# Kernel optimization log

Measured on AMD Instinct MI355X. Metric: run time of the kernel, lower is better.

Reference implementation:

```python
import jax, jax.numpy as jnp
import numpy as np
from jax import lax

B, T, NI = 1024, 16, 11

def skew(v):  # [...,3,1] -> [...,3,3]
    x, y, z = v[..., 0, 0], v[..., 1, 0], v[..., 2, 0]
    o = jnp.zeros_like(x)
    return jnp.stack([jnp.stack([o, -z, y], -1),
                      jnp.stack([z, o, -x], -1),
                      jnp.stack([-y, x, o], -1)], -2)

def exp_SO3(phi):  # [...,3,1] -> [...,3,3] (Rodrigues, safe small-angle)
    t2 = jnp.sum(phi * phi, axis=(-2, -1))[..., None, None]
    small = t2 < 1e-8
    t2s = jnp.where(small, 1.0, t2)
    t = jnp.sqrt(t2s)
    A = jnp.where(small, 1.0 - t2 / 6.0, jnp.sin(t) / t)
    Bc = jnp.where(small, 0.5 - t2 / 24.0, (1.0 - jnp.cos(t)) / t2s)
    K = skew(phi)
    return jnp.eye(3, dtype=phi.dtype) + A * K + Bc * (K @ K)

def log_SO3(C):  # [...,3,3] -> [...,3,1]
    tr = jnp.trace(C, axis1=-2, axis2=-1)[..., None, None]
    c = jnp.clip((tr - 1.0) * 0.5, -1.0 + 1e-7, 1.0 - 1e-7)
    t = jnp.arccos(c)
    small = t < 1e-4
    s = jnp.where(small, 1.0, jnp.sin(t))
    coef = jnp.where(small, 0.5 + t * t / 12.0, t / (2.0 * s))
    S = coef * (C - jnp.swapaxes(C, -1, -2))
    return jnp.stack([S[..., 2, 1], S[..., 0, 2], S[..., 1, 0]], -1)[..., None]

def J_left_inv(phi):  # inverse left Jacobian of SO(3)
    t2 = jnp.sum(phi * phi, axis=(-2, -1))[..., None, None]
    small = t2 < 1e-8
    t2s = jnp.where(small, 1.0, t2)
    t = jnp.sqrt(t2s)
    coef = jnp.where(small, 1.0 / 12.0,
                     1.0 / t2s - (1.0 + jnp.cos(t)) / (2.0 * t * jnp.sin(t)))
    K = skew(phi)
    return jnp.eye(3, dtype=phi.dtype) - 0.5 * K + coef * (K @ K)

def decode(s):
    b = s.shape[0]
    return (s[:, 0:3].reshape(b, 3, 1), s[:, 3:12].reshape(b, 3, 3),
            s[:, 12:15].reshape(b, 3, 1), s[:, 15:18].reshape(b, 3, 1),
            s[:, 18:21].reshape(b, 3, 1), s[:, 21:24].reshape(b, 3, 1),
            s[:, 24].reshape(b, 1, 1))

def encode(g, C, r, v, bw, ba, lambd):
    b = g.shape[0]
    return jnp.concatenate([g.reshape(b, 3), C.reshape(b, 9), r.reshape(b, 3),
                            v.reshape(b, 3), bw.reshape(b, 3), ba.reshape(b, 3),
                            lambd.reshape(b, 1)], -1)

def force_sym(M):
    u = jnp.triu(M)
    return u + jnp.swapaxes(u, -1, -2) * (1.0 - jnp.eye(M.shape[-1], dtype=M.dtype))

def predict_one_step(t_acc, C_acc, r_acc, v_acc, dt, g_k, v_k, bw_k, ba_k, covar, gyro, accel, Rimu):
    b = dt.shape[0]
    dt2 = dt * dt
    w = gyro - bw_k
    w_sk = skew(w)
    C_T = jnp.swapaxes(C_acc, -1, -2)
    a = accel - ba_k
    v = C_T @ (v_k - g_k * t_acc + v_acc)
    v_sk = skew(v)
    I3 = jnp.eye(3, dtype=dt.dtype)
    E = exp_SO3(dt * w)
    E_T = jnp.swapaxes(E, -1, -2)
    F = jnp.zeros((b, 19, 19), dt.dtype)
    F = F.at[:, 3:6, 3:6].set(-w_sk)
    F = F.at[:, 3:6, 12:15].set(-I3)
    F = F.at[:, 6:9, 3:6].set(-(C_acc @ v_sk))
    F = F.at[:, 6:9, 9:12].set(C_acc)
    F = F.at[:, 9:12, 0:3].set(-C_T)
    F = F.at[:, 9:12, 3:6].set(-skew(C_T @ g_k))
    F = F.at[:, 9:12, 9:12].set(-w_sk)
    F = F.at[:, 9:12, 12:15].set(-v_sk)
    F = F.at[:, 9:12, 15:18].set(-I3)
    G = jnp.zeros((b, 19, 12), dt.dtype)
    G = G.at[:, 3:6, 0:3].set(-I3)
    G = G.at[:, 9:12, 0:3].set(-v_sk)
    G = G.at[:, 9:12, 6:9].set(-I3)
    G = G.at[:, 12:15, 3:6].set(I3)
    G = G.at[:, 15:18, 9:12].set(I3)
    Phi = jnp.eye(19, dtype=dt.dtype) + F * dt + 0.5 * (F @ F) * dt2
    Phi = Phi.at[:, 6:9, 12:15].set(0.0)
    Phi = Phi.at[:, 3:6, 3:6].set(E_T)
    Phi = Phi.at[:, 9:12, 9:12].set(E_T)
    PhiG = Phi @ G
    Q = (PhiG @ Rimu @ jnp.swapaxes(PhiG, -1, -2)) * dt
    covar = force_sym(Phi @ covar @ jnp.swapaxes(Phi, -1, -2) + Q)
    r_acc = r_acc + v_acc * dt + 0.5 * (C_acc @ (dt2 * a))
    v_acc = v_acc + C_acc @ (dt * a)
    C_acc = C_acc @ E
    t_acc = t_acc + dt
    return t_acc, C_acc, r_acc, v_acc, covar

def predict(imu_meas, Rimu, prev_state, prev_covar):
    b = imu_meas.shape[0]
    dtype = prev_covar.dtype
    g_k, _, _, v_k, bw_k, ba_k, lambd = decode(prev_state)
    u = jnp.array([1.0] * 3 + [0.0] * 6 + [1.0] * 10, dtype)
    covar = prev_covar * (u[:, None] * u[None, :])  # U P U^T with diagonal U
    t = imu_meas[..., 0]
    gyro = imu_meas[..., 1:4][..., None]
    accel = imu_meas[..., 4:7][..., None]
    dt = (t[:, 1:] - t[:, :-1])[..., None, None]
    init = (jnp.zeros((b, 1, 1), dtype),
            jnp.tile(jnp.eye(3, dtype=dtype), (b, 1, 1)),
            jnp.zeros((b, 3, 1), dtype), jnp.zeros((b, 3, 1), dtype), covar)
    xs = (jnp.swapaxes(dt, 0, 1), jnp.swapaxes(gyro[:, :-1], 0, 1), jnp.swapaxes(accel[:, :-1], 0, 1))
    def step(c, x):
        t_acc, C_acc, r_acc, v_acc, cov = c
        dt_, gy, ac = x
        return predict_one_step(t_acc, C_acc, r_acc, v_acc, dt_, g_k, v_k, bw_k, ba_k, cov, gy, ac, Rimu), None
    (t_acc, C_acc, r_acc, v_acc, cov), _ = lax.scan(step, init, xs)
    pred_state = encode(g_k, C_acc,
                        v_k * t_acc - 0.5 * g_k * t_acc * t_acc + r_acc,
                        jnp.swapaxes(C_acc, -1, -2) @ (v_k - g_k * t_acc + v_acc),
                        bw_k, ba_k, lambd)
    return pred_state, cov

def update(pred_state, pred_covar, vis_meas, vis_meas_covar):
    b = pred_state.shape[0]
    dtype = pred_state.dtype
    g_p, C_p, r_p, v_p, bw_p, ba_p, l_p = decode(pred_state)
    phi = log_SO3(C_p)
    residual = jnp.concatenate([vis_meas[:, 0:3] - phi, vis_meas[:, 3:6] - l_p * r_p], 1)
    H = jnp.zeros((b, 6, 19), dtype)
    H = H.at[:, 0:3, 3:6].set(-J_left_inv(-phi))
    H = H.at[:, 3:6, 6:9].set(-jnp.eye(3, dtype=dtype) * l_p)
    H = H.at[:, 3:6, 18:19].set(-r_p)
    H = -H
    H_T = jnp.swapaxes(H, -1, -2)
    S = H @ pred_covar @ H_T + vis_meas_covar
    K = pred_covar @ H_T @ jnp.linalg.inv(S)
    e = K @ residual
    est_covar = (jnp.eye(19, dtype=dtype) - K @ H) @ pred_covar
    est_state = encode(g_p + e[:, 0:3], C_p @ exp_SO3(e[:, 3:6]), r_p + e[:, 6:9],
                       v_p + e[:, 9:12], bw_p + e[:, 12:15], ba_p + e[:, 15:18],
                       l_p + e[:, 18:19])
    return est_state, est_covar

def composition(prev_pose, est_state, est_covar):
    b = est_state.shape[0]
    dtype = est_state.dtype
    g, C, r, v, bw, ba, lambd = decode(est_state)
    C_T = jnp.swapaxes(C, -1, -2)
    pose = jnp.tile(jnp.eye(4, dtype=dtype), (b, 1, 1))
    pose = pose.at[:, 0:3, 0:3].set(C_T @ prev_pose[:, 0:3, 0:3])
    pose = pose.at[:, 0:3, 3:4].set(C_T @ (prev_pose[:, 0:3, 3:4] - r))
    new_g = C_T @ g
    new_state = encode(new_g, C, r, v, bw, ba, lambd)
    U = jnp.tile(jnp.eye(19, dtype=dtype), (b, 1, 1))
    U = U.at[:, 0:3, 0:3].set(C_T)
    U = U.at[:, 0:3, 3:6].set(skew(new_g))
    new_covar = force_sym(U @ est_covar @ jnp.swapaxes(U, -1, -2))
    return pose, new_state, new_covar

def setup_inputs() -> dict:
    key = jax.random.key(0)
    k1, k2, k3 = jax.random.split(key, 3)
    dtype = jnp.float32
    times = jnp.broadcast_to(jnp.arange(NI, dtype=dtype) * 0.01, (B, T, NI))
    gyro = jax.random.normal(k1, (B, T, NI, 3), dtype) * 0.05
    accel = jax.random.normal(k2, (B, T, NI, 3), dtype) * 0.1
    imu_data = jnp.concatenate([times[..., None], gyro, accel], -1)  # [B,T,NI,7]
    imu_noise_covar = jnp.eye(12, dtype=dtype) * 1e-4
    prev_pose = jnp.tile(jnp.eye(4, dtype=dtype), (B, 1, 1))
    g0 = jnp.array([0.0, 0.0, 9.81], dtype)
    C0 = jnp.eye(3, dtype=dtype).reshape(9)
    prev_state = jnp.broadcast_to(
        jnp.concatenate([g0, C0, jnp.zeros(12, dtype), jnp.ones(1, dtype)]), (B, 25))
    prev_covar = jnp.tile(jnp.eye(19, dtype=dtype) * 1e-2, (B, 1, 1))
    vis_meas = jax.random.normal(k3, (B, T, 6, 1), dtype) * 0.01
    vis_meas_covar = jnp.tile(jnp.eye(6, dtype=dtype) * 1e-2, (B, T, 1, 1))
    T_imu_cam = jnp.tile(jnp.eye(4, dtype=dtype), (B, 1, 1))
    return dict(imu_data=imu_data, imu_noise_covar=imu_noise_covar, prev_pose=prev_pose,
                prev_state=prev_state, prev_covar=prev_covar, vis_meas=vis_meas,
                vis_meas_covar=vis_meas_covar, T_imu_cam=T_imu_cam)

def reference(imu_data, imu_noise_covar, prev_pose, prev_state, prev_covar, vis_meas, vis_meas_covar, T_imu_cam):
    num_timesteps = vis_meas.shape[1]
    poses, states, covars = [prev_pose], [prev_state], [prev_covar]
    for k in range(num_timesteps):
        ps, pc = predict(imu_data[:, k], imu_noise_covar, states[-1], covars[-1])
        es, ec = update(ps, pc, vis_meas[:, k], vis_meas_covar[:, k])
        npo, ns, nc = composition(poses[-1], es, ec)
        poses.append(npo); states.append(ns); covars.append(nc)
    return (jnp.stack(poses, 1), jnp.stack(states, 1), jnp.stack(covars, 1))
```

## Files before the change

### kernel.cpp

```cpp
#include <hip/hip_runtime.h>

#define NB 1024
#define NT 16
#define NIM 11
#define PIT 20
#define NTH 128

struct __align__(16) SharedBlob {
    float P0[19*PIT];
    float P1[19*PIT];
    float A9[9*PIT];
    float Dall[10][9*PIT];
    float Wsall[10][9*12];
    float Wu[19*12];
    float Mu[19*12];
    float T[3*PIT];
    float Rd[12];
    float sqRd[12];
    float Aug[2][84];
    float E[20];
    float dts[12];
    unsigned short tri[192];
};

__device__ __forceinline__ float sel3(int i, float a, float b, float c){
    return i==0 ? a : (i==1 ? b : c);
}
__device__ __forceinline__ void skew3(float x, float y, float z, float K[9]) {
    K[0]=0.f;  K[1]=-z;   K[2]=y;
    K[3]=z;    K[4]=0.f;  K[5]=-x;
    K[6]=-y;   K[7]=x;    K[8]=0.f;
}
__device__ __forceinline__ void mm3(const float A[9], const float Bm[9], float C[9]) {
#pragma unroll
    for (int i=0;i<3;i++)
#pragma unroll
        for (int j=0;j<3;j++)
            C[i*3+j] = A[i*3+0]*Bm[0+j] + A[i*3+1]*Bm[3+j] + A[i*3+2]*Bm[6+j];
}
__device__ __forceinline__ void exp_SO3f(float p0, float p1, float p2, float R[9]) {
    float t2 = p0*p0+p1*p1+p2*p2;
    bool sm = t2 < 1e-8f;
    float t2s = sm ? 1.0f : t2;
    float t = sqrtf(t2s);
    float sn, cs; __sincosf(t, &sn, &cs);
    float A = sm ? (1.0f - t2*(1.0f/6.0f)) : (sn/t);
    float Bc = sm ? (0.5f - t2*(1.0f/24.0f)) : ((1.0f - cs)/t2s);
    float K[9]; skew3(p0,p1,p2,K);
    float K2[9]; mm3(K,K,K2);
#pragma unroll
    for (int i=0;i<9;i++) R[i] = A*K[i] + Bc*K2[i];
    R[0]+=1.f; R[4]+=1.f; R[8]+=1.f;
}
__device__ __forceinline__ void log_SO3(const float C[9], float p[3]) {
    float tr = C[0]+C[4]+C[8];
    float c = (tr-1.0f)*0.5f;
    c = fminf(fmaxf(c, -1.0f+1e-7f), 1.0f-1e-7f);
    float t = acosf(c);
    bool sm = t < 1e-4f;
    float s = sm ? 1.0f : sinf(t);
    float coef = sm ? (0.5f + t*t*(1.0f/12.0f)) : (t/(2.0f*s));
    p[0] = coef*(C[7]-C[5]);
    p[1] = coef*(C[2]-C[6]);
    p[2] = coef*(C[3]-C[1]);
}
__device__ __forceinline__ void J_left_inv(const float p[3], float J[9]) {
    float t2 = p[0]*p[0]+p[1]*p[1]+p[2]*p[2];
    bool sm = t2 < 1e-8f;
    float t2s = sm ? 1.0f : t2;
    float t = sqrtf(t2s);
    float coef = sm ? (1.0f/12.0f) : (1.0f/t2s - (1.0f+cosf(t))/(2.0f*t*sinf(t)));
    float K[9]; skew3(p[0],p[1],p[2],K);
    float K2[9]; mm3(K,K,K2);
#pragma unroll
    for (int i=0;i<9;i++) J[i] = -0.5f*K[i] + coef*K2[i];
    J[0]+=1.f; J[4]+=1.f; J[8]+=1.f;
}
__device__ __forceinline__ float dot12_rr(const float* a, const float* b){
    const float4* a4=(const float4*)a;
    const float4* b4=(const float4*)b;
    float s=0.f;
#pragma unroll
    for (int q=0;q<3;q++){
        float4 x=a4[q], y=b4[q];
        s += x.x*y.x + x.y*y.y + x.z*y.z + x.w*y.w;
    }
    return s;
}
__device__ __forceinline__ float dotD(const float* Ai, const float* Dr, int jb){
    float s = Ai[3]*Dr[3]+Ai[4]*Dr[4]+Ai[5]*Dr[5];
    if (jb==0){
        s += Ai[12]*Dr[12]+Ai[13]*Dr[13]+Ai[14]*Dr[14];
    } else {
        s += Ai[0]*Dr[0]+Ai[1]*Dr[1]+Ai[2]*Dr[2]
           + Ai[9]*Dr[9]+Ai[10]*Dr[10]+Ai[11]*Dr[11]
           + Ai[15]*Dr[15]+Ai[16]*Dr[16]+Ai[17]*Dr[17];
        if (jb==2) s += Ai[12]*Dr[12]+Ai[13]*Dr[13]+Ai[14]*Dr[14];
    }
    return s;
}

__global__ void __launch_bounds__(NTH, 2) kf_kernel(
    const float* __restrict__ imu_data,
    const float* __restrict__ Rimu,
    const float* __restrict__ prev_pose,
    const float* __restrict__ prev_state,
    const float* __restrict__ prev_covar,
    const float* __restrict__ vis_meas,
    const float* __restrict__ vis_covar,
    float* __restrict__ out_poses,
    float* __restrict__ out_states,
    float* __restrict__ out_covars)
{
    __shared__ SharedBlob S;
    const int t = threadIdx.x;
    const int b = blockIdx.x;
    const int w = t >> 6;
    const int l = t & 63;

    const float* pcv = prev_covar + (size_t)b*361;
    for (int e=t;e<361;e+=NTH){
        float v = pcv[e];
        int i=e/19, j=e%19;
        bool msk = (i>=3&&i<9)||(j>=3&&j<9);
        S.P0[i*PIT + j] = msk ? 0.f : v;
        out_covars[((size_t)b*17)*361 + e] = v;
    }
    for (int e=t;e<10*9*PIT;e+=NTH) S.Dall[0][e] = 0.f;
    if (t<12){ float rv = Rimu[t*12+t]; S.Rd[t]=rv; S.sqRd[t]=sqrtf(rv); }
    if (t<16) out_poses[((size_t)b*17)*16 + t] = prev_pose[(size_t)b*16+t];
    if (t<25) out_states[((size_t)b*17)*25 + t] = prev_state[(size_t)b*25+t];
    for (int e=t;e<190;e+=NTH){
        int i=0, rem=e;
        while (rem >= 19-i){ rem -= 19-i; i++; }
        S.tri[e] = (unsigned short)((i<<5)|(i+rem));
    }

    const float* st = prev_state + (size_t)b*25;
    float g0=st[0], g1=st[1], g2=st[2];
    float vk0=st[15], vk1=st[16], vk2=st[17];
    float bw0=st[18], bw1=st[19], bw2=st[20];
    float ba0=st[21], ba1=st[22], ba2=st[23];
    float lam=st[24];
    const float* pp = prev_pose + (size_t)b*16;
    float pR[9] = {pp[0],pp[1],pp[2], pp[4],pp[5],pp[6], pp[8],pp[9],pp[10]};
    float pT0=pp[3], pT1=pp[7], pT2=pp[11];

    __syncthreads();

    for (int k=0;k<NT;k++){
        float Cc[9] = {1,0,0, 0,1,0, 0,0,1};
        float ra0=0,ra1=0,ra2=0, va0=0,va1=0,va2=0, tac=0;
        const float* imu = imu_data + ((size_t)b*NT + k)*NIM*7;

        for (int s=0;s<NIM-1;s++){
            const float* m0 = imu + s*7;
            float dt = m0[7] - m0[0];
            float w0=m0[1]-bw0, w1=m0[2]-bw1, w2=m0[3]-bw2;
            float a0=m0[4]-ba0, a1=m0[5]-ba1, a2=m0[6]-ba2;
            float u0=vk0-g0*tac+va0, u1=vk1-g1*tac+va1, u2=vk2-g2*tac+va2;
            float vv0=Cc[0]*u0+Cc[3]*u1+Cc[6]*u2;
            float vv1=Cc[1]*u0+Cc[4]*u1+Cc[7]*u2;
            float vv2=Cc[2]*u0+Cc[5]*u1+Cc[8]*u2;
            float ct0=Cc[0]*g0+Cc[3]*g1+Cc[6]*g2;
            float ct1=Cc[1]*g0+Cc[4]*g1+Cc[7]*g2;
            float ct2=Cc[2]*g0+Cc[5]*g1+Cc[8]*g2;
            float Em[9]; exp_SO3f(dt*w0, dt*w1, dt*w2, Em);
            float hdt2 = 0.5f*dt*dt;

            if (t<27){
                int r=t/9, ii=(t%9)/3, jj=t%3;
                float dij = (ii==jj)?1.f:0.f;
                int o = ii*PIT + jj;
                float* Dp = S.Dall[s];
                if (r==0){
                    float eJ0=sel3(jj,Em[0],Em[3],Em[6]), eJ1=sel3(jj,Em[1],Em[4],Em[7]), eJ2=sel3(jj,Em[2],Em[5],Em[8]);
                    float EmTIJ = sel3(ii,eJ0,eJ1,eJ2);
                    float wcJ0=sel3(jj,0.f,-w2,w1), wcJ1=sel3(jj,w2,0.f,-w0), wcJ2=sel3(jj,-w1,w0,0.f);
                    float wskIJ = sel3(ii,wcJ0,wcJ1,wcJ2);
                    Dp[o+3]  = EmTIJ - dij;
                    Dp[o+12] = -dt*dij + hdt2*wskIJ;
                } else if (r==1){
                    float cI0=sel3(ii,Cc[0],Cc[3],Cc[6]), cI1=sel3(ii,Cc[1],Cc[4],Cc[7]), cI2=sel3(ii,Cc[2],Cc[5],Cc[8]);
                    float cJ0=sel3(jj,Cc[0],Cc[3],Cc[6]), cJ1=sel3(jj,Cc[1],Cc[4],Cc[7]), cJ2=sel3(jj,Cc[2],Cc[5],Cc[8]);
                    float ccJ0=sel3(jj,Cc[0],Cc[1],Cc[2]), ccJ1=sel3(jj,Cc[3],Cc[4],Cc[5]), ccJ2=sel3(jj,Cc[6],Cc[7],Cc[8]);
                    float CIJ = sel3(ii,ccJ0,ccJ1,ccJ2);
                    float vcJ0=sel3(jj,0.f,-vv2,vv1), vcJ1=sel3(jj,vv2,0.f,-vv0), vcJ2=sel3(jj,-vv1,vv0,0.f);
                    float tcJ0=sel3(jj,0.f,-ct2,ct1), tcJ1=sel3(jj,ct2,0.f,-ct0), tcJ2=sel3(jj,-ct1,ct0,0.f);
                    float wcJ0=sel3(jj,0.f,-w2,w1), wcJ1=sel3(jj,w2,0.f,-w0), wcJ2=sel3(jj,-w1,w0,0.f);
                    float CCtIJ  = cI0*cJ0 + cI1*cJ1 + cI2*cJ2;
                    float CvskIJ = cI0*vcJ0 + cI1*vcJ1 + cI2*vcJ2;
                    float Cv0 =  cI1*vv2 - cI2*vv1;
                    float Cv1 = -cI0*vv2 + cI2*vv0;
                    float Cv2 =  cI0*vv1 - cI1*vv0;
                    float CvwIJ = Cv0*wcJ0 + Cv1*wcJ1 + Cv2*wcJ2;
                    float CctIJ = cI0*tcJ0 + cI1*tcJ1 + cI2*tcJ2;
                    float CwIJ  = cI0*wcJ0 + cI1*wcJ1 + cI2*wcJ2;
                    Dp[3*PIT + o + 0]  = -hdt2*CCtIJ;
                    Dp[3*PIT + o + 3]  = -dt*CvskIJ + hdt2*(CvwIJ - CctIJ);
                    Dp[3*PIT + o + 9]  =  dt*CIJ - hdt2*CwIJ;
                    Dp[3*PIT + o + 15] = -hdt2*CIJ;
                } else {
                    float cJ0=sel3(jj,Cc[0],Cc[3],Cc[6]), cJ1=sel3(jj,Cc[1],Cc[4],Cc[7]), cJ2=sel3(jj,Cc[2],Cc[5],Cc[8]);
                    float CTIJ = sel3(ii,cJ0,cJ1,cJ2);
                    float eJ0=sel3(jj,Em[0],Em[3],Em[6]), eJ1=sel3(jj,Em[1],Em[4],Em[7]), eJ2=sel3(jj,Em[2],Em[5],Em[8]);
                    float EmTIJ = sel3(ii,eJ0,eJ1,eJ2);
                    float wrI0=sel3(ii,0.f,w2,-w1), wrI1=sel3(ii,-w2,0.f,w0), wrI2=sel3(ii,w1,-w0,0.f);
                    float wcJ0=sel3(jj,0.f,-w2,w1), wcJ1=sel3(jj,w2,0.f,-w0), wcJ2=sel3(jj,-w1,w0,0.f);
                    float wskIJ = sel3(ii,wcJ0,wcJ1,wcJ2);
                    float vcJ0=sel3(jj,0.f,-vv2,vv1), vcJ1=sel3(jj,vv2,0.f,-vv0), vcJ2=sel3(jj,-vv1,vv0,0.f);
                    float vskIJ = sel3(ii,vcJ0,vcJ1,vcJ2);
                    float trI0=sel3(ii,0.f,ct2,-ct1), trI1=sel3(ii,-ct2,0.f,ct0), trI2=sel3(ii,ct1,-ct0,0.f);
                    float tcJ0=sel3(jj,0.f,-ct2,ct1), tcJ1=sel3(jj,ct2,0.f,-ct0), tcJ2=sel3(jj,-ct1,ct0,0.f);
                    float ctskIJ = sel3(ii,tcJ0,tcJ1,tcJ2);
                    float wCtIJ = wrI0*cJ0 + wrI1*cJ1 + wrI2*cJ2;
                    float ctwIJ = trI0*wcJ0 + trI1*wcJ1 + trI2*wcJ2;
                    float wctIJ = wrI0*tcJ0 + wrI1*tcJ1 + wrI2*tcJ2;
                    float wvIJ  = wrI0*vcJ0 + wrI1*vcJ1 + wrI2*vcJ2;
                    Dp[6*PIT + o + 0]  = -dt*CTIJ + hdt2*wCtIJ;
                    Dp[6*PIT + o + 3]  = -dt*ctskIJ + hdt2*(ctwIJ + wctIJ);
                    Dp[6*PIT + o + 9]  = EmTIJ - dij;
                    Dp[6*PIT + o + 12] = -dt*vskIJ + hdt2*(ctskIJ + wvIJ);
                    Dp[6*PIT + o + 15] = -dt*dij + hdt2*wskIJ;
                }
            }
            if (t==3) S.dts[s] = dt;
            if (w==0){
                __builtin_amdgcn_wave_barrier();
                asm volatile("s_waitcnt lgkmcnt(0)" ::: "memory");
                __builtin_amdgcn_wave_barrier();
                float* Wp = S.Wsall[s];
                const float* Dp2 = S.Dall[s];
                for (int e=l;e<108;e+=64){
                    int i=e/12, j=e%12;
                    const float* Dr = &Dp2[i*PIT];
                    int ri = 3+i;
                    float val;
                    if (j<3){
                        float v0j = sel3(j, 0.f, -vv2,  vv1);
                        float v1j = sel3(j, vv2,  0.f, -vv0);
                        float v2j = sel3(j,-vv1,  vv0,  0.f);
                        val = -((ri==3+j)?1.f:0.f) - Dr[3+j]
                              - (((ri==9 )?1.f:0.f)+Dr[9 ])*v0j
                              - (((ri==10)?1.f:0.f)+Dr[10])*v1j
                              - (((ri==11)?1.f:0.f)+Dr[11])*v2j;
                    } else if (j<6) val = Dr[9+j];
                    else if (j<9) val = -(((ri==j+3)?1.f:0.f) + Dr[j+3]);
                    else val = Dr[6+j];
                    Wp[i*12+j] = val * S.sqRd[j];
                }
            }

            float d2 = dt*dt;
            float e0=d2*a0, e1=d2*a1, e2=d2*a2;
            ra0 += va0*dt + 0.5f*(Cc[0]*e0+Cc[1]*e1+Cc[2]*e2);
            ra1 += va1*dt + 0.5f*(Cc[3]*e0+Cc[4]*e1+Cc[5]*e2);
            ra2 += va2*dt + 0.5f*(Cc[6]*e0+Cc[7]*e1+Cc[8]*e2);
            float da0=dt*a0, da1=dt*a1, da2=dt*a2;
            va0 += Cc[0]*da0+Cc[1]*da1+Cc[2]*da2;
            va1 += Cc[3]*da0+Cc[4]*da1+Cc[5]*da2;
            va2 += Cc[6]*da0+Cc[7]*da1+Cc[8]*da2;
            float Cn[9]; mm3(Cc, Em, Cn);
#pragma unroll
            for (int q=0;q<9;q++) Cc[q]=Cn[q];
            tac += dt;
        }
        __syncthreads();

        for (int s=0;s<NIM-1;s++){
            float* Pc = (s&1) ? S.P1 : S.P0;
            float* Pn = (s&1) ? S.P0 : S.P1;
            const float* Ds = S.Dall[s];
            const float* Wss = S.Wsall[s];
            float dt = S.dts[s];

            int aBeg = (w==0)?0:57, aEnd = (w==0)?57:171;
            for (int e=aBeg+l;e<aEnd;e+=64){
                int i=e/19, j=e%19;
                const float* Dr = &Ds[i*PIT];
                float s2 = Pc[(3+i)*PIT+j]
                         + Dr[0]*Pc[0*PIT+j]+Dr[1]*Pc[1*PIT+j]+Dr[2]*Pc[2*PIT+j]
                         + Dr[3]*Pc[3*PIT+j]+Dr[4]*Pc[4*PIT+j]+Dr[5]*Pc[5*PIT+j]
                         + Dr[9]*Pc[9*PIT+j]+Dr[10]*Pc[10*PIT+j]+Dr[11]*Pc[11*PIT+j]
                         + Dr[12]*Pc[12*PIT+j]+Dr[13]*Pc[13*PIT+j]+Dr[14]*Pc[14*PIT+j]
                         + Dr[15]*Pc[15*PIT+j]+Dr[16]*Pc[16*PIT+j]+Dr[17]*Pc[17*PIT+j];
                S.A9[i*PIT+j]=s2;
            }
            __builtin_amdgcn_wave_barrier();
            asm volatile("s_waitcnt lgkmcnt(0)" ::: "memory");
            __builtin_amdgcn_wave_barrier();

            int tBase = (w==0)?0:99, tCnt = (w==0)?99:91;
            for (int e2=l;e2<tCnt;e2+=64){
                int tt=S.tri[tBase+e2]; int i=tt>>5, j=tt&31;
                const float* Ai = (i>=3 && i<12) ? &S.A9[(i-3)*PIT] : &Pc[i*PIT];
                float val = Ai[j];
                if (j>=3 && j<12) val += dotD(Ai, &Ds[(j-3)*PIT], (j-3)/3);
                if (i>=3){
                    if (j<12) val += dt*dot12_rr(&Wss[(i-3)*12], &Wss[(j-3)*12]);
                    else if (i<12){
                        if (j<15) val += dt*Wss[(i-3)*12 + (j-9)]*S.sqRd[j-9];
                        else if (j<18) val += dt*Wss[(i-3)*12 + (j-6)]*S.sqRd[j-6];
                    } else if (i==j){
                        if (i<15) val += dt*S.Rd[i-9];
                        else if (i<18) val += dt*S.Rd[i-6];
                    }
                }
                Pn[i*PIT+j]=val; Pn[j*PIT+i]=val;
            }
            __syncthreads();
        }

        float t2a = tac*tac;
        float rp0 = vk0*tac - 0.5f*g0*t2a + ra0;
        float rp1 = vk1*tac - 0.5f*g1*t2a + ra1;
        float rp2 = vk2*tac - 0.5f*g2*t2a + ra2;
        float u0=vk0-g0*tac+va0, u1=vk1-g1*tac+va1, u2=vk2-g2*tac+va2;
        float vpr0=Cc[0]*u0+Cc[3]*u1+Cc[6]*u2;
        float vpr1=Cc[1]*u0+Cc[4]*u1+Cc[7]*u2;
        float vpr2=Cc[2]*u0+Cc[5]*u1+Cc[8]*u2;

        float phi[3]; log_SO3(Cc, phi);
        float nphi[3]={-phi[0],-phi[1],-phi[2]};
        float Jli[9]; J_left_inv(nphi, Jli);
        const float* vm = vis_meas + ((size_t)b*NT+k)*6;
        float res0=vm[0]-phi[0], res1=vm[1]-phi[1], res2=vm[2]-phi[2];
        float res3=vm[3]-lam*rp0, res4=vm[4]-lam*rp1, res5=vm[5]-lam*rp2;

        if (t<114){
            int i=t/6, j=t%6;
            float val;
            if (j<3){
                float jr0 = sel3(j, Jli[0], Jli[3], Jli[6]);
                float jr1 = sel3(j, Jli[1], Jli[4], Jli[7]);
                float jr2 = sel3(j, Jli[2], Jli[5], Jli[8]);
                val = S.P0[i*PIT+3]*jr0 + S.P0[i*PIT+4]*jr1 + S.P0[i*PIT+5]*jr2;
            } else {
                float rsel = sel3(j-3, rp0, rp1, rp2);
                val = lam*S.P0[i*PIT+6+(j-3)] + rsel*S.P0[i*PIT+18];
            }
            S.Wu[i*12+j]=val;
        }
        __syncthreads();
        const float* vmc = vis_covar + ((size_t)b*NT+k)*36;
        if (t<84){
            int i=t/14, c=t%14;
            float val;
            if (c<6){
                float hp;
                if (i<3){
                    float jr0 = sel3(i, Jli[0], Jli[3], Jli[6]);
                    float jr1 = sel3(i, Jli[1], Jli[4], Jli[7]);
                    float jr2 = sel3(i, Jli[2], Jli[5], Jli[8]);
                    hp = jr0*S.Wu[3*12+c]+jr1*S.Wu[4*12+c]+jr2*S.Wu[5*12+c];
                } else {
                    float rsel = sel3(i-3, rp0, rp1, rp2);
                    hp = lam*S.Wu[(3+i)*12+c] + rsel*S.Wu[18*12+c];
                }
                val = hp + vmc[i*6+c];
            } else val = ((c-6)==i)?1.f:0.f;
            S.Aug[0][i*14+c]=val;
        }
        __syncthreads();
        if (t<64){
            int i0=t/14, c0=t%14;
            int e1=t+64, i1=e1/14, c1=e1%14;
            bool h1 = e1<84;
            int cur=0;
#pragma unroll
            for (int kk=0;kk<6;kk++){
                const float* Ac = S.Aug[cur];
                float* An = S.Aug[cur^1];
                float rpv = 1.0f/Ac[kk*14+kk];
                float piv0 = Ac[kk*14+c0]*rpv;
                float nv0 = (i0==kk)? piv0 : (Ac[i0*14+c0] - Ac[i0*14+kk]*piv0);
                float nv1 = 0.f;
                if (h1){
                    float piv1 = Ac[kk*14+c1]*rpv;
                    nv1 = (i1==kk)? piv1 : (Ac[i1*14+c1] - Ac[i1*14+kk]*piv1);
                }
                An[i0*14+c0]=nv0;
                if (h1) An[i1*14+c1]=nv1;
                cur^=1;
                __builtin_amdgcn_wave_barrier();
            }
        }
        __syncthreads();
        if (t<114){
            int i=t/6, j=t%6;
            float s2=0.f;
#pragma unroll
            for (int m=0;m<6;m++) s2 += S.Wu[i*12+m]*S.Aug[0][m*14+6+j];
            S.Mu[i*12+j]=s2;
        }
        __syncthreads();
        for (int e=t;e<133;e+=NTH){
            int i=e/7, c=e%7;
            float val;
            if (c<3){
                float jc0 = sel3(c, Jli[0], Jli[1], Jli[2]);
                float jc1 = sel3(c, Jli[3], Jli[4], Jli[5]);
                float jc2 = sel3(c, Jli[6], Jli[7], Jli[8]);
                val = S.Mu[i*12+0]*jc0 + S.Mu[i*12+1]*jc1 + S.Mu[i*12+2]*jc2;
            }
            else if (c<6) val = S.Mu[i*12+c]*lam;
            else val = S.Mu[i*12+3]*rp0 + S.Mu[i*12+4]*rp1 + S.Mu[i*12+5]*rp2;
            S.Wu[i*12+c]=val;
        }
        if (t<19){
            S.E[t] = S.Mu[t*12+0]*res0 + S.Mu[t*12+1]*res1 + S.Mu[t*12+2]*res2
                   + S.Mu[t*12+3]*res3 + S.Mu[t*12+4]*res4 + S.Mu[t*12+5]*res5;
        }
        __syncthreads();
        for (int e=t;e<361;e+=NTH){
            int i=e/19, j=e%19;
            float s2 = S.P0[i*PIT+j];
#pragma unroll
            for (int c=0;c<6;c++) s2 -= S.Wu[i*12+c]*S.P0[(3+c)*PIT+j];
            s2 -= S.Wu[i*12+6]*S.P0[18*PIT+j];
            S.P1[i*PIT+j]=s2;
        }
        float ev[19];
#pragma unroll
        for (int q=0;q<19;q++) ev[q]=S.E[q];
        g0+=ev[0]; g1+=ev[1]; g2+=ev[2];
        float dE[9]; exp_SO3f(ev[3], ev[4], ev[5], dE);
        float Ce[9]; mm3(Cc,dE,Ce);
        float re0=rp0+ev[6], re1=rp1+ev[7], re2=rp2+ev[8];
        float vE0=vpr0+ev[9], vE1=vpr1+ev[10], vE2=vpr2+ev[11];
        bw0+=ev[12]; bw1+=ev[13]; bw2+=ev[14];
        ba0+=ev[15]; ba1+=ev[16]; ba2+=ev[17];
        lam+=ev[18];
        float gn0=Ce[0]*g0+Ce[3]*g1+Ce[6]*g2;
        float gn1=Ce[1]*g0+Ce[4]*g1+Ce[7]*g2;
        float gn2=Ce[2]*g0+Ce[5]*g1+Ce[8]*g2;
        float Rn[9];
#pragma unroll
        for (int i=0;i<3;i++)
#pragma unroll
            for (int j=0;j<3;j++)
                Rn[i*3+j] = Ce[0*3+i]*pR[0*3+j] + Ce[1*3+i]*pR[1*3+j] + Ce[2*3+i]*pR[2*3+j];
        float dv0=pT0-re0, dv1=pT1-re1, dv2=pT2-re2;
        float Tn0=Ce[0]*dv0+Ce[3]*dv1+Ce[6]*dv2;
        float Tn1=Ce[1]*dv0+Ce[4]*dv1+Ce[7]*dv2;
        float Tn2=Ce[2]*dv0+Ce[5]*dv1+Ce[8]*dv2;
        __syncthreads();
        if (t<57){
            int i=t/19, j=t%19;
            float c0 = sel3(i, Ce[0], Ce[1], Ce[2]);
            float c1 = sel3(i, Ce[3], Ce[4], Ce[5]);
            float c2 = sel3(i, Ce[6], Ce[7], Ce[8]);
            float gs0 = sel3(i, 0.f,  gn2, -gn1);
            float gs1 = sel3(i, -gn2, 0.f,  gn0);
            float gs2 = sel3(i, gn1, -gn0,  0.f);
            float val = c0*S.P1[0*PIT+j] + c1*S.P1[1*PIT+j] + c2*S.P1[2*PIT+j]
                      + gs0*S.P1[3*PIT+j] + gs1*S.P1[4*PIT+j] + gs2*S.P1[5*PIT+j];
            S.T[i*PIT+j]=val;
        }
        __syncthreads();
        size_t obase = (size_t)b*17 + (size_t)(k+1);
        for (int e=t;e<190;e+=NTH){
            int tt=S.tri[e]; int i=tt>>5, j=tt&31;
            float val;
            if (j<3){
                float c0 = sel3(j, Ce[0], Ce[1], Ce[2]);
                float c1 = sel3(j, Ce[3], Ce[4], Ce[5]);
                float c2 = sel3(j, Ce[6], Ce[7], Ce[8]);
                float gs0 = sel3(j, 0.f,  gn2, -gn1);
                float gs1 = sel3(j, -gn2, 0.f,  gn0);
                float gs2 = sel3(j, gn1, -gn0,  0.f);
                val = S.T[i*PIT+0]*c0 + S.T[i*PIT+1]*c1 + S.T[i*PIT+2]*c2
                    + S.T[i*PIT+3]*gs0 + S.T[i*PIT+4]*gs1 + S.T[i*PIT+5]*gs2;
            } else {
                val = (i<3) ? S.T[i*PIT+j] : S.P1[i*PIT+j];
            }
            bool msk = (i>=3&&i<9)||(j>=3&&j<9);
            float pv = msk ? 0.f : val;
            S.P0[i*PIT+j]=pv; S.P0[j*PIT+i]=pv;
            out_covars[obase*361 + i*19 + j] = val;
            if (i!=j) out_covars[obase*361 + j*19 + i] = val;
        }
        if (t==0){
            float* po = out_poses + obase*16;
            po[0]=Rn[0]; po[1]=Rn[1]; po[2]=Rn[2];  po[3]=Tn0;
            po[4]=Rn[3]; po[5]=Rn[4]; po[6]=Rn[5];  po[7]=Tn1;
            po[8]=Rn[6]; po[9]=Rn[7]; po[10]=Rn[8]; po[11]=Tn2;
            po[12]=0.f; po[13]=0.f; po[14]=0.f; po[15]=1.f;
            float* so = out_states + obase*25;
            so[0]=gn0; so[1]=gn1; so[2]=gn2;
#pragma unroll
            for (int q=0;q<9;q++) so[3+q]=Ce[q];
            so[12]=re0; so[13]=re1; so[14]=re2;
            so[15]=vE0; so[16]=vE1; so[17]=vE2;
            so[18]=bw0; so[19]=bw1; so[20]=bw2;
            so[21]=ba0; so[22]=ba1; so[23]=ba2;
            so[24]=lam;
        }
        g0=gn0; g1=gn1; g2=gn2;
        vk0=vE0; vk1=vE1; vk2=vE2;
#pragma unroll
        for (int q=0;q<9;q++) pR[q]=Rn[q];
        pT0=Tn0; pT1=Tn1; pT2=Tn2;
        __syncthreads();
    }
}

extern "C" void kernel_launch(void* const* d_in, const int* in_sizes, int n_in,
                              void* d_out, int out_size, void* d_ws, size_t ws_size,
                              hipStream_t stream) {
    const float* imu    = (const float*)d_in[0];
    const float* Rimu   = (const float*)d_in[1];
    const float* ppose  = (const float*)d_in[2];
    const float* pstate = (const float*)d_in[3];
    const float* pcov   = (const float*)d_in[4];
    const float* vm     = (const float*)d_in[5];
    const float* vmc    = (const float*)d_in[6];
    float* out = (float*)d_out;
    float* out_poses  = out;
    float* out_states = out + (size_t)NB*17*16;
    float* out_covars = out + (size_t)NB*17*16 + (size_t)NB*17*25;
    hipLaunchKernelGGL(kf_kernel, dim3(NB), dim3(NTH), 0, stream,
        imu, Rimu, ppose, pstate, pcov, vm, vmc, out_poses, out_states, out_covars);
}
```

Baseline: 612.0 us.

## Map one batch element per wavefront, replacing block barriers with wave syncs

Each 128-thread block now handles two batch elements, one per 64-lane wavefront, each with its own shared-memory blob. All __syncthreads are replaced with wave-local barriers plus an LDS wait, and work previously split across two waves is done by one wave in strided loops. This removes block-wide barrier stalls in the long serial Kalman recurrence, at the cost of twice the LDS per block and more serial work per wave.

```diff
diff --git a/kernel.cpp b/kernel.cpp
--- a/kernel.cpp
+++ b/kernel.cpp
@@ -5,6 +5,10 @@
 #define NIM 11
 #define PIT 20
 #define NTH 128
+
+#define WSYNC() do { __builtin_amdgcn_wave_barrier(); \
+                     asm volatile("s_waitcnt lgkmcnt(0)" ::: "memory"); \
+                     __builtin_amdgcn_wave_barrier(); } while(0)
 
 struct __align__(16) SharedBlob {
     float P0[19*PIT];
@@ -112,25 +116,26 @@
     float* __restrict__ out_states,
     float* __restrict__ out_covars)
 {
-    __shared__ SharedBlob S;
-    const int t = threadIdx.x;
-    const int b = blockIdx.x;
-    const int w = t >> 6;
-    const int l = t & 63;
+    __shared__ SharedBlob SS[2];
+    const int tid = threadIdx.x;
+    const int w   = tid >> 6;
+    const int l   = tid & 63;
+    const int b   = blockIdx.x*2 + w;
+    SharedBlob& S = SS[w];
 
     const float* pcv = prev_covar + (size_t)b*361;
-    for (int e=t;e<361;e+=NTH){
+    for (int e=l;e<361;e+=64){
         float v = pcv[e];
         int i=e/19, j=e%19;
         bool msk = (i>=3&&i<9)||(j>=3&&j<9);
         S.P0[i*PIT + j] = msk ? 0.f : v;
         out_covars[((size_t)b*17)*361 + e] = v;
     }
-    for (int e=t;e<10*9*PIT;e+=NTH) S.Dall[0][e] = 0.f;
-    if (t<12){ float rv = Rimu[t*12+t]; S.Rd[t]=rv; S.sqRd[t]=sqrtf(rv); }
-    if (t<16) out_poses[((size_t)b*17)*16 + t] = prev_pose[(size_t)b*16+t];
-    if (t<25) out_states[((size_t)b*17)*25 + t] = prev_state[(size_t)b*25+t];
-    for (int e=t;e<190;e+=NTH){
+    for (int e=l;e<10*9*PIT;e+=64) S.Dall[0][e] = 0.f;
+    if (l<12){ float rv = Rimu[l*12+l]; S.Rd[l]=rv; S.sqRd[l]=sqrtf(rv); }
+    if (l<16) out_poses[((size_t)b*17)*16 + l] = prev_pose[(size_t)b*16+l];
+    if (l<25) out_states[((size_t)b*17)*25 + l] = prev_state[(size_t)b*25+l];
+    for (int e=l;e<190;e+=64){
         int i=0, rem=e;
         while (rem >= 19-i){ rem -= 19-i; i++; }
         S.tri[e] = (unsigned short)((i<<5)|(i+rem));
@@ -146,7 +151,7 @@
     float pR[9] = {pp[0],pp[1],pp[2], pp[4],pp[5],pp[6], pp[8],pp[9],pp[10]};
     float pT0=pp[3], pT1=pp[7], pT2=pp[11];
 
-    __syncthreads();
+    WSYNC();
 
     for (int k=0;k<NT;k++){
         float Cc[9] = {1,0,0, 0,1,0, 0,0,1};
@@ -168,8 +173,8 @@
             float Em[9]; exp_SO3f(dt*w0, dt*w1, dt*w2, Em);
             float hdt2 = 0.5f*dt*dt;
 
-            if (t<27){
-                int r=t/9, ii=(t%9)/3, jj=t%3;
+            if (l<27){
+                int r=l/9, ii=(l%9)/3, jj=l%3;
                 float dij = (ii==jj)?1.f:0.f;
                 int o = ii*PIT + jj;
                 float* Dp = S.Dall[s];
@@ -224,11 +229,9 @@
                     Dp[6*PIT + o + 15] = -dt*dij + hdt2*wskIJ;
                 }
             }
-            if (t==3) S.dts[s] = dt;
-            if (w==0){
-                __builtin_amdgcn_wave_barrier();
-                asm volatile("s_waitcnt lgkmcnt(0)" ::: "memory");
-                __builtin_amdgcn_wave_barrier();
+            if (l==3) S.dts[s] = dt;
+            WSYNC();
+            {
                 float* Wp = S.Wsall[s];
                 const float* Dp2 = S.Dall[s];
                 for (int e=l;e<108;e+=64){
@@ -265,7 +268,7 @@
             for (int q=0;q<9;q++) Cc[q]=Cn[q];
             tac += dt;
         }
-        __syncthreads();
+        WSYNC();
 
         for (int s=0;s<NIM-1;s++){
             float* Pc = (s&1) ? S.P1 : S.P0;
@@ -274,8 +277,7 @@
             const float* Wss = S.Wsall[s];
             float dt = S.dts[s];
 
-            int aBeg = (w==0)?0:57, aEnd = (w==0)?57:171;
-            for (int e=aBeg+l;e<aEnd;e+=64){
+            for (int e=l;e<171;e+=64){
                 int i=e/19, j=e%19;
                 const float* Dr = &Ds[i*PIT];
                 float s2 = Pc[(3+i)*PIT+j]
@@ -286,13 +288,10 @@
                          + Dr[15]*Pc[15*PIT+j]+Dr[16]*Pc[16*PIT+j]+Dr[17]*Pc[17*PIT+j];
                 S.A9[i*PIT+j]=s2;
             }
-            __builtin_amdgcn_wave_barrier();
-            asm volatile("s_waitcnt lgkmcnt(0)" ::: "memory");
-            __builtin_amdgcn_wave_barrier();
-
-            int tBase = (w==0)?0:99, tCnt = (w==0)?99:91;
-            for (int e2=l;e2<tCnt;e2+=64){
-                int tt=S.tri[tBase+e2]; int i=tt>>5, j=tt&31;
+            WSYNC();
+
+            for (int e2=l;e2<190;e2+=64){
+                int tt=S.tri[e2]; int i=tt>>5, j=tt&31;
                 const float* Ai = (i>=3 && i<12) ? &S.A9[(i-3)*PIT] : &Pc[i*PIT];
                 float val = Ai[j];
                 if (j>=3 && j<12) val += dotD(Ai, &Ds[(j-3)*PIT], (j-3)/3);
@@ -308,7 +307,7 @@
                 }
                 Pn[i*PIT+j]=val; Pn[j*PIT+i]=val;
             }
-            __syncthreads();
+            WSYNC();
         }
 
         float t2a = tac*tac;
@@ -327,8 +326,8 @@
         float res0=vm[0]-phi[0], res1=vm[1]-phi[1], res2=vm[2]-phi[2];
         float res3=vm[3]-lam*rp0, res4=vm[4]-lam*rp1, res5=vm[5]-lam*rp2;
 
-        if (t<114){
-            int i=t/6, j=t%6;
+        for (int e=l;e<114;e+=64){
+            int i=e/6, j=e%6;
             float val;
             if (j<3){
                 float jr0 = sel3(j, Jli[0], Jli[3], Jli[6]);
@@ -341,10 +340,10 @@
             }
             S.Wu[i*12+j]=val;
         }
-        __syncthreads();
+        WSYNC();
         const float* vmc = vis_covar + ((size_t)b*NT+k)*36;
-        if (t<84){
-            int i=t/14, c=t%14;
+        for (int e=l;e<84;e+=64){
+            int i=e/14, c=e%14;
             float val;
             if (c<6){
                 float hp;
@@ -361,10 +360,10 @@
             } else val = ((c-6)==i)?1.f:0.f;
             S.Aug[0][i*14+c]=val;
         }
-        __syncthreads();
-        if (t<64){
-            int i0=t/14, c0=t%14;
-            int e1=t+64, i1=e1/14, c1=e1%14;
+        WSYNC();
+        {
+            int i0=l/14, c0=l%14;
+            int e1=l+64, i1=e1/14, c1=e1%14;
             bool h1 = e1<84;
             int cur=0;
 #pragma unroll
@@ -385,16 +384,16 @@
                 __builtin_amdgcn_wave_barrier();
             }
         }
-        __syncthreads();
-        if (t<114){
-            int i=t/6, j=t%6;
+        WSYNC();
+        for (int e=l;e<114;e+=64){
+            int i=e/6, j=e%6;
             float s2=0.f;
 #pragma unroll
             for (int m=0;m<6;m++) s2 += S.Wu[i*12+m]*S.Aug[0][m*14+6+j];
             S.Mu[i*12+j]=s2;
         }
-        __syncthreads();
-        for (int e=t;e<133;e+=NTH){
+        WSYNC();
+        for (int e=l;e<133;e+=64){
             int i=e/7, c=e%7;
             float val;
             if (c<3){
@@ -407,12 +406,12 @@
             else val = S.Mu[i*12+3]*rp0 + S.Mu[i*12+4]*rp1 + S.Mu[i*12+5]*rp2;
             S.Wu[i*12+c]=val;
         }
-        if (t<19){
-            S.E[t] = S.Mu[t*12+0]*res0 + S.Mu[t*12+1]*res1 + S.Mu[t*12+2]*res2
-                   + S.Mu[t*12+3]*res3 + S.Mu[t*12+4]*res4 + S.Mu[t*12+5]*res5;
-        }
-        __syncthreads();
-        for (int e=t;e<361;e+=NTH){
+        if (l<19){
+            S.E[l] = S.Mu[l*12+0]*res0 + S.Mu[l*12+1]*res1 + S.Mu[l*12+2]*res2
+                   + S.Mu[l*12+3]*res3 + S.Mu[l*12+4]*res4 + S.Mu[l*12+5]*res5;
+        }
+        WSYNC();
+        for (int e=l;e<361;e+=64){
             int i=e/19, j=e%19;
             float s2 = S.P0[i*PIT+j];
 #pragma unroll
@@ -444,9 +443,9 @@
         float Tn0=Ce[0]*dv0+Ce[3]*dv1+Ce[6]*dv2;
         float Tn1=Ce[1]*dv0+Ce[4]*dv1+Ce[7]*dv2;
         float Tn2=Ce[2]*dv0+Ce[5]*dv1+Ce[8]*dv2;
-        __syncthreads();
-        if (t<57){
-            int i=t/19, j=t%19;
+        WSYNC();
+        if (l<57){
+            int i=l/19, j=l%19;
             float c0 = sel3(i, Ce[0], Ce[1], Ce[2]);
             float c1 = sel3(i, Ce[3], Ce[4], Ce[5]);
             float c2 = sel3(i, Ce[6], Ce[7], Ce[8]);
@@ -457,9 +456,9 @@
                       + gs0*S.P1[3*PIT+j] + gs1*S.P1[4*PIT+j] + gs2*S.P1[5*PIT+j];
             S.T[i*PIT+j]=val;
         }
-        __syncthreads();
+        WSYNC();
         size_t obase = (size_t)b*17 + (size_t)(k+1);
-        for (int e=t;e<190;e+=NTH){
+        for (int e=l;e<190;e+=64){
             int tt=S.tri[e]; int i=tt>>5, j=tt&31;
             float val;
             if (j<3){
@@ -480,7 +479,7 @@
             out_covars[obase*361 + i*19 + j] = val;
             if (i!=j) out_covars[obase*361 + j*19 + i] = val;
         }
-        if (t==0){
+        if (l==0){
             float* po = out_poses + obase*16;
             po[0]=Rn[0]; po[1]=Rn[1]; po[2]=Rn[2];  po[3]=Tn0;
             po[4]=Rn[3]; po[5]=Rn[4]; po[6]=Rn[5];  po[7]=Tn1;
@@ -501,7 +500,7 @@
 #pragma unroll
         for (int q=0;q<9;q++) pR[q]=Rn[q];
         pT0=Tn0; pT1=Tn1; pT2=Tn2;
-        __syncthreads();
+        WSYNC();
     }
 }
 
@@ -519,6 +518,6 @@
     float* out_poses  = out;
     float* out_states = out + (size_t)NB*17*16;
     float* out_covars = out + (size_t)NB*17*16 + (size_t)NB*17*25;
-    hipLaunchKernelGGL(kf_kernel, dim3(NB), dim3(NTH), 0, stream,
+    hipLaunchKernelGGL(kf_kernel, dim3(NB/2), dim3(NTH), 0, stream,
         imu, Rimu, ppose, pstate, pcov, vm, vmc, out_poses, out_states, out_covars);
 }
```

Result: slower. 857.9 us (+40.2%).
